# Performance work log

Measured on AMD Instinct MI355X. Metric: run time of the kernel, lower is better.

The kernel has to match this reference:

```python
import jax, jax.numpy as jnp
import numpy as np

NEG = -1e30  # log(0) surrogate that stays finite in fp32
BLANK = 0


def setup_inputs() -> dict:
    key = jax.random.key(0)
    k1, k2 = jax.random.split(key)
    B, T, V, L = 32, 1024, 1024, 256
    logits = jax.random.normal(k1, (B, T, V), dtype=jnp.float32)
    log_probs = jax.nn.log_softmax(logits, axis=-1)  # module expects log-probs
    labels = jax.random.randint(k2, (B, L), 1, V, dtype=jnp.int32)  # avoid blank=0
    input_lens = jnp.full((B,), T, dtype=jnp.int32)
    label_lens = jnp.full((B,), L, dtype=jnp.int32)
    return {"log_probs": log_probs, "labels": labels,
            "input_lens": input_lens, "label_lens": label_lens}


def _ctc_loss_sum(log_probs, labels, input_lens, label_lens, blank=BLANK):
    """CTC forward DP (alpha recursion) in log space; reduction='sum', zero_infinity=True."""
    B, T, V = log_probs.shape
    L = labels.shape[1]
    S = 2 * L + 1  # extended label: blank l1 blank l2 ... blank

    ext = jnp.full((B, S), blank, dtype=labels.dtype)
    ext = ext.at[:, 1::2].set(labels)
    # skip transition s-2 -> s allowed iff ext[s] != blank and ext[s] != ext[s-2]
    skip = jnp.concatenate(
        [jnp.zeros((B, 2), dtype=bool),
         (ext[:, 2:] != blank) & (ext[:, 2:] != ext[:, :-2])], axis=1)

    lp_tbv = jnp.transpose(log_probs, (1, 0, 2))  # 'btv->tbv' as in the module

    emit0 = jnp.take_along_axis(lp_tbv[0], ext, axis=1)  # [B,S]
    alpha0 = jnp.full((B, S), NEG, dtype=log_probs.dtype)
    alpha0 = alpha0.at[:, 0].set(emit0[:, 0]).at[:, 1].set(emit0[:, 1])

    neg1 = jnp.full((B, 1), NEG, dtype=log_probs.dtype)
    neg2 = jnp.full((B, 2), NEG, dtype=log_probs.dtype)

    def step(alpha, inputs):
        lp_t, t = inputs  # lp_t: [B,V]
        em = jnp.take_along_axis(lp_t, ext, axis=1)  # [B,S]
        a1 = alpha
        a2 = jnp.concatenate([neg1, alpha[:, :-1]], axis=1)
        a3 = jnp.where(skip, jnp.concatenate([neg2, alpha[:, :-2]], axis=1), NEG)
        new = jnp.logaddexp(jnp.logaddexp(a1, a2), a3) + em
        # freeze alpha once past this sample's input length
        new = jnp.where((t < input_lens)[:, None], new, alpha)
        return new, None

    ts = jnp.arange(1, T)
    alpha, _ = jax.lax.scan(step, alpha0, (lp_tbv[1:], ts))

    s_last = 2 * label_lens  # final blank state index per sample
    a_last = jnp.take_along_axis(alpha, s_last[:, None], axis=1)[:, 0]
    a_prev = jnp.take_along_axis(alpha, (s_last - 1)[:, None], axis=1)[:, 0]
    loss_b = -jnp.logaddexp(a_last, a_prev)
    loss_b = jnp.where(loss_b > 1e29, 0.0, loss_b)  # zero_infinity=True
    return jnp.sum(loss_b)


def reference(log_probs, labels, input_lens, label_lens):
    return _ctc_loss_sum(log_probs, labels, input_lens, label_lens)
```

## Files before the change

kernel.cpp:

```cpp
#include <hip/hip_runtime.h>


constexpr int B_ = 32, T_ = 1024, V_ = 1024, L_ = 256;
constexpr int CH = 16;
constexpr int NCHUNK = 64;
constexpr int NBUF = 4;
constexpr float LN2F = 0.6931471805599453f;

typedef const __attribute__((address_space(1))) unsigned int* gp_t;
typedef __attribute__((address_space(3))) unsigned int* lp_t;

template <int CTRL>
__device__ __forceinline__ float dpp_fmax(float x) {
    const int t = __builtin_amdgcn_update_dpp(0, __float_as_int(x), CTRL, 0xf, 0xf, true);
    return fmaxf(x, __int_as_float(t));
}

__device__ __forceinline__ float wave_max_dpp(float x) {
    x = dpp_fmax<0x111>(x);
    x = dpp_fmax<0x112>(x);
    x = dpp_fmax<0x114>(x);
    x = dpp_fmax<0x118>(x);
    x = dpp_fmax<0x142>(x);
    x = dpp_fmax<0x143>(x);
    return __int_as_float(__builtin_amdgcn_readlane(__float_as_int(x), 63));
}

__device__ __forceinline__ float dpp_wave_shr1(float x) {
    return __int_as_float(
        __builtin_amdgcn_update_dpp(0, __float_as_int(x), 0x138, 0xf, 0xf, true));
}

__global__ __launch_bounds__(256, 8) void ctc_gather(
    const float* __restrict__ lp, float* __restrict__ qdst, int qstride,
    const int* __restrict__ labels, float* __restrict__ blanks)
{
    __shared__ float srow[4][V_];
    const int wave = threadIdx.x >> 6;
    const int lane = threadIdx.x & 63;
    const int r = blockIdx.x * 4 + wave;
    const int b = r >> 10;
    const float* row = lp + (size_t)r * V_;
    float* orow = qdst + (size_t)r * qstride;
    const int* labb = labels + b * L_;

    #pragma unroll
    for (int j = 0; j < 4; ++j)
        __builtin_amdgcn_global_load_lds((gp_t)(row + 256 * j + 4 * lane),
                                         (lp_t)&srow[wave][256 * j], 16, 0, 0);
    const int4 e = *(const int4*)(labb + 4 * lane);
    asm volatile("s_waitcnt vmcnt(0)" ::: "memory");
    __builtin_amdgcn_sched_barrier(0);
    const float v0 = srow[wave][e.x];
    const float v1 = srow[wave][e.y];
    const float v2 = srow[wave][e.z];
    const float v3 = srow[wave][e.w];
    const float vb = srow[wave][0];
    float4 q;
    q.x = __expf(v0); q.y = __expf(v1); q.z = __expf(v2); q.w = __expf(v3);
    const float qb = __expf(vb);
    *(float4*)(orow + 4 * lane) = q;
    if (lane == 0) {
        const int t = r & (T_ - 1);
        blanks[(r & ~(T_ - 1)) + ((t + T_ - 1) & (T_ - 1))] = qb;
    }
}

__global__ __launch_bounds__(64, 1) void ctc_dp(
    const float* __restrict__ Q, int qstride,
    const float* __restrict__ blanks, const int* __restrict__ labels,
    const int* __restrict__ input_lens, const int* __restrict__ label_lens,
    float* __restrict__ out)
{
    __shared__ float blk[T_];
    __shared__ float buf[NBUF][CH][256];
    const int b    = blockIdx.x;
    const int lane = threadIdx.x & 63;
    const float* Qb  = Q + (size_t)b * T_ * qstride;
    const float* blg = blanks + b * T_;
    const int*  labb = labels + b * L_;
    const int il = input_lens[b];
    const int ll = label_lens[b];
    const int tend = il < T_ ? il : T_;

    auto issue_chunk = [&](int c) {
        #pragma unroll
        for (int i = 0; i < CH; ++i) {
            int t = 1 + c * CH + i; if (t > T_ - 1) t = T_ - 1;
            __builtin_amdgcn_global_load_lds(
                (gp_t)(Qb + (size_t)t * qstride + 4 * lane),
                (lp_t)&buf[c & (NBUF - 1)][i][0], 16, 0, 0);
        }
    };

    #pragma unroll
    for (int i = 0; i < 4; ++i)
        __builtin_amdgcn_global_load_lds((gp_t)(blg + 256 * i + 4 * lane),
                                         (lp_t)&blk[256 * i], 16, 0, 0);
    issue_chunk(0); issue_chunk(1); issue_chunk(2);

    const int4 e  = *(const int4*)(labb + 4 * lane);
    const int  ep = (lane > 0) ? labb[4 * lane - 1] : -1;
    const float kf0 = ((8 * lane + 1) >= 3 && e.x != ep) ? 1.f : 0.f;
    const float kf1 = (e.y != e.x) ? 1.f : 0.f;
    const float kf2 = (e.z != e.y) ? 1.f : 0.f;
    const float kf3 = (e.w != e.z) ? 1.f : 0.f;
    const float bl0 = blg[T_ - 1];
    const float q00 = Qb[0];
    float p0 = (lane == 0) ? bl0 : 0.f;
    float p1 = (lane == 0) ? q00 : 0.f;
    float p2 = 0.f, p3 = 0.f, p4 = 0.f, p5 = 0.f,
          p6 = 0.f, p7 = 0.f, p8 = 0.f;
    int Esc = 0;
    float pm1 = 0.f;
    float sfP = 1.f, sfM = 1.f;

    asm volatile("s_waitcnt vmcnt(32)" ::: "memory");
    __builtin_amdgcn_sched_barrier(0);

    auto snap = [&]() -> float {
        float m = fmaxf(fmaxf(fmaxf(fmaxf(p0, p1), fmaxf(p2, p3)),
                              fmaxf(fmaxf(p4, p5), fmaxf(p6, p7))), p8);
        m = wave_max_dpp(m);
        const unsigned eb = (__float_as_uint(m) >> 23) & 0xffu;
        if (eb >= 1u && eb <= 254u) {
            unsigned k = 318u - eb;
            if (k > 254u) k = 254u;
            Esc += (int)k - 127;
            return __uint_as_float(k << 23);
        }
        return 1.f;
    };

    for (int c = 0; c < NCHUNK; ++c) {
        if (c + 3 < NCHUNK) {
            issue_chunk(c + 3);
            asm volatile("s_waitcnt vmcnt(32)" ::: "memory");
        } else if (c == NCHUNK - 3) {
            asm volatile("s_waitcnt vmcnt(16)" ::: "memory");
        } else if (c == NCHUNK - 2) {
            asm volatile("s_waitcnt vmcnt(0)"  ::: "memory");
        }
        __builtin_amdgcn_sched_barrier(0);

        const float* base = &buf[c & (NBUF - 1)][0][0] + 4 * lane;
        float4 qv[CH];
        #pragma unroll
        for (int i = 0; i < CH; ++i)
            qv[i] = *(const float4*)(base + 256 * i);
        float bb[CH];
        #pragma unroll
        for (int i = 0; i < CH; i += 4) {
            const float4 t4 = *(const float4*)&blk[c * CH + i];
            bb[i] = t4.x; bb[i + 1] = t4.y;
            bb[i + 2] = t4.z; bb[i + 3] = t4.w;
        }
        #pragma unroll
        for (int i = 0; i < CH; ++i) {
            float4 q = qv[i];
            float qb = bb[i];
            if (i == 0) { q.x *= sfP; q.y *= sfP; q.z *= sfP; q.w *= sfP; qb *= sfP; }
            if (i == 8) { q.x *= sfM; q.y *= sfM; q.z *= sfM; q.w *= sfM; qb *= sfM; }
            const int t = 1 + c * CH + i;
            if (t < tend) {
                const float n7 = fmaf(kf3, p5, p7 + p6) * q.w;
                const float n8 = (p8 + p7) * qb;
                const float pm1n = dpp_wave_shr1(n7);
                const float n0 = (p0 + pm1) * qb;
                const float n1 = fmaf(kf0, pm1, p1 + p0) * q.x;
                const float n2 = (p2 + p1) * qb;
                const float n3 = fmaf(kf1, p1, p3 + p2) * q.y;
                const float n4 = (p4 + p3) * qb;
                const float n5 = fmaf(kf2, p3, p5 + p4) * q.z;
                const float n6 = (p6 + p5) * qb;
                p0 = n0; p1 = n1; p2 = n2; p3 = n3; p4 = n4;
                p5 = n5; p6 = n6; p7 = n7; p8 = n8; pm1 = pm1n;
            }
            if (i == 4)  sfM = snap();
            if (i == 12) sfP = snap();
        }
    }
    p0 *= sfP; p1 *= sfP; p2 *= sfP; p3 *= sfP; p4 *= sfP;
    p5 *= sfP; p6 *= sfP; p7 *= sfP; p8 *= sfP;

    const int sl = 2 * ll;
    auto pick = [&](int s) -> float {
        if (s == 512) return __shfl(p8, 63);
        const int r = s & 7;
        float v = p0;
        v = (r == 1) ? p1 : v; v = (r == 2) ? p2 : v;
        v = (r == 3) ? p3 : v; v = (r == 4) ? p4 : v;
        v = (r == 5) ? p5 : v; v = (r == 6) ? p6 : v;
        v = (r == 7) ? p7 : v;
        return __shfl(v, s >> 3);
    };
    const float la = pick(sl);
    const float lb = pick(sl - 1);
    if (lane == 0) {
        const float tot = la + lb;
        float loss = (float)Esc * LN2F - __logf(tot);
        if (!(loss <= 1e29f)) loss = 0.f;
        atomicAdd(out, loss);
    }
}

extern "C" void kernel_launch(void* const* d_in, const int* in_sizes, int n_in,
                              void* d_out, int out_size, void* d_ws, size_t ws_size,
                              hipStream_t stream) {
    float*       lp     = (float*)d_in[0];
    const int*   labels = (const int*)d_in[1];
    const int*   il     = (const int*)d_in[2];
    const int*   ll     = (const int*)d_in[3];
    float* out    = (float*)d_out;
    float* blanks = (float*)d_ws;

    const size_t need = (size_t)B_ * T_ * sizeof(float)
                      + (size_t)B_ * T_ * 256 * sizeof(float);
    const bool use_ws = ws_size >= need;
    float* qdst = use_ws ? (blanks + (size_t)B_ * T_) : lp;
    const int qstride = use_ws ? 256 : V_;

    hipMemsetAsync(out, 0, sizeof(float), stream);
    ctc_gather<<<dim3(B_ * T_ / 4), dim3(256), 0, stream>>>(
        lp, qdst, qstride, labels, blanks);
    ctc_dp<<<dim3(B_), dim3(64), 0, stream>>>(
        qdst, qstride, blanks, labels, il, ll, out);
}
```

Measured before the change: 299.5 us.

## Split DP kernel into producer waves and consumer wave with LDS flag handshake

The DP block grows from one wave to five. Four producer waves load chunks of gathered probabilities from global memory into LDS ring slots, and a single consumer wave runs the serial recurrence, synchronising through workgroup-scope acquire/release flags. This takes the global-load issue and waitcnt stalls off the latency-critical recurrence wave. In exchange it adds spin-wait polling on LDS atomics, register round-trips for the loads instead of direct global-to-LDS transfers, and extra waves competing for issue slots.

```diff
diff --git a/kernel.cpp b/kernel.cpp
--- a/kernel.cpp
+++ b/kernel.cpp
@@ -5,6 +5,7 @@
 constexpr int CH = 16;
 constexpr int NCHUNK = 64;
 constexpr int NBUF = 4;
+constexpr int PROD = 4;
 constexpr float LN2F = 0.6931471805599453f;
 
 typedef const __attribute__((address_space(1))) unsigned int* gp_t;
@@ -66,7 +67,7 @@
     }
 }
 
-__global__ __launch_bounds__(64, 1) void ctc_dp(
+__global__ __launch_bounds__(320, 1) void ctc_dp(
     const float* __restrict__ Q, int qstride,
     const float* __restrict__ blanks, const int* __restrict__ labels,
     const int* __restrict__ input_lens, const int* __restrict__ label_lens,
@@ -74,8 +75,12 @@
 {
     __shared__ float blk[T_];
     __shared__ float buf[NBUF][CH][256];
+    __shared__ int Pf[NBUF];
+    __shared__ int Cf;
     const int b    = blockIdx.x;
-    const int lane = threadIdx.x & 63;
+    const int tid  = threadIdx.x;
+    const int lane = tid & 63;
+    const int wv   = tid >> 6;
     const float* Qb  = Q + (size_t)b * T_ * qstride;
     const float* blg = blanks + b * T_;
     const int*  labb = labels + b * L_;
@@ -83,124 +88,136 @@
     const int ll = label_lens[b];
     const int tend = il < T_ ? il : T_;
 
-    auto issue_chunk = [&](int c) {
+    if (tid < NBUF) Pf[tid] = 0;
+    if (tid == NBUF) Cf = 0;
+    __syncthreads();
+
+    if (wv < PROD) {
+        for (int c = wv; c < NCHUNK; c += PROD) {
+            if (c >= NBUF) {
+                while (__hip_atomic_load(&Cf, __ATOMIC_ACQUIRE,
+                                         __HIP_MEMORY_SCOPE_WORKGROUP)
+                       < c - (NBUF - 1)) {}
+            }
+            float4 r[CH];
+            #pragma unroll
+            for (int i = 0; i < CH; ++i) {
+                int t = 1 + c * CH + i; if (t > T_ - 1) t = T_ - 1;
+                r[i] = *(const float4*)(Qb + (size_t)t * qstride + 4 * lane);
+            }
+            float* dst = &buf[wv][0][0] + 4 * lane;
+            #pragma unroll
+            for (int i = 0; i < CH; ++i)
+                *(float4*)(dst + 256 * i) = r[i];
+            if (lane == 0)
+                __hip_atomic_store(&Pf[wv], c + 1, __ATOMIC_RELEASE,
+                                   __HIP_MEMORY_SCOPE_WORKGROUP);
+        }
+    } else {
         #pragma unroll
-        for (int i = 0; i < CH; ++i) {
-            int t = 1 + c * CH + i; if (t > T_ - 1) t = T_ - 1;
-            __builtin_amdgcn_global_load_lds(
-                (gp_t)(Qb + (size_t)t * qstride + 4 * lane),
-                (lp_t)&buf[c & (NBUF - 1)][i][0], 16, 0, 0);
+        for (int i = 0; i < 4; ++i)
+            __builtin_amdgcn_global_load_lds((gp_t)(blg + 256 * i + 4 * lane),
+                                             (lp_t)&blk[256 * i], 16, 0, 0);
+
+        const int4 e  = *(const int4*)(labb + 4 * lane);
+        const int  ep = (lane > 0) ? labb[4 * lane - 1] : -1;
+        const float kf0 = ((8 * lane + 1) >= 3 && e.x != ep) ? 1.f : 0.f;
+        const float kf1 = (e.y != e.x) ? 1.f : 0.f;
+        const float kf2 = (e.z != e.y) ? 1.f : 0.f;
+        const float kf3 = (e.w != e.z) ? 1.f : 0.f;
+        const float bl0 = blg[T_ - 1];
+        const float q00 = Qb[0];
+        float p0 = (lane == 0) ? bl0 : 0.f;
+        float p1 = (lane == 0) ? q00 : 0.f;
+        float p2 = 0.f, p3 = 0.f, p4 = 0.f, p5 = 0.f,
+              p6 = 0.f, p7 = 0.f, p8 = 0.f;
+        int Esc = 0;
+        float pm1 = 0.f;
+        float sfP = 1.f, sfM = 1.f;
+
+        asm volatile("s_waitcnt vmcnt(0)" ::: "memory");
+        __builtin_amdgcn_sched_barrier(0);
+
+        auto snap = [&]() -> float {
+            float m = fmaxf(fmaxf(fmaxf(fmaxf(p0, p1), fmaxf(p2, p3)),
+                                  fmaxf(fmaxf(p4, p5), fmaxf(p6, p7))), p8);
+            m = wave_max_dpp(m);
+            const unsigned eb = (__float_as_uint(m) >> 23) & 0xffu;
+            if (eb >= 1u && eb <= 254u) {
+                unsigned k = 318u - eb;
+                if (k > 254u) k = 254u;
+                Esc += (int)k - 127;
+                return __uint_as_float(k << 23);
+            }
+            return 1.f;
+        };
+
+        for (int c = 0; c < NCHUNK; ++c) {
+            const int slot = c & (NBUF - 1);
+            while (__hip_atomic_load(&Pf[slot], __ATOMIC_ACQUIRE,
+                                     __HIP_MEMORY_SCOPE_WORKGROUP) < c + 1) {}
+            const float* base = &buf[slot][0][0] + 4 * lane;
+            float4 qv[CH];
+            #pragma unroll
+            for (int i = 0; i < CH; ++i)
+                qv[i] = *(const float4*)(base + 256 * i);
+            float bb[CH];
+            #pragma unroll
+            for (int i = 0; i < CH; i += 4) {
+                const float4 t4 = *(const float4*)&blk[c * CH + i];
+                bb[i] = t4.x; bb[i + 1] = t4.y;
+                bb[i + 2] = t4.z; bb[i + 3] = t4.w;
+            }
+            if (lane == 0)
+                __hip_atomic_store(&Cf, c + 1, __ATOMIC_RELEASE,
+                                   __HIP_MEMORY_SCOPE_WORKGROUP);
+            #pragma unroll
+            for (int i = 0; i < CH; ++i) {
+                float4 q = qv[i];
+                float qb = bb[i];
+                if (i == 0) { q.x *= sfP; q.y *= sfP; q.z *= sfP; q.w *= sfP; qb *= sfP; }
+                if (i == 8) { q.x *= sfM; q.y *= sfM; q.z *= sfM; q.w *= sfM; qb *= sfM; }
+                const int t = 1 + c * CH + i;
+                if (t < tend) {
+                    const float n7 = fmaf(kf3, p5, p7 + p6) * q.w;
+                    const float n8 = (p8 + p7) * qb;
+                    const float pm1n = dpp_wave_shr1(n7);
+                    const float n0 = (p0 + pm1) * qb;
+                    const float n1 = fmaf(kf0, pm1, p1 + p0) * q.x;
+                    const float n2 = (p2 + p1) * qb;
+                    const float n3 = fmaf(kf1, p1, p3 + p2) * q.y;
+                    const float n4 = (p4 + p3) * qb;
+                    const float n5 = fmaf(kf2, p3, p5 + p4) * q.z;
+                    const float n6 = (p6 + p5) * qb;
+                    p0 = n0; p1 = n1; p2 = n2; p3 = n3; p4 = n4;
+                    p5 = n5; p6 = n6; p7 = n7; p8 = n8; pm1 = pm1n;
+                }
+                if (i == 4)  sfM = snap();
+                if (i == 12) sfP = snap();
+            }
         }
-    };
-
-    #pragma unroll
-    for (int i = 0; i < 4; ++i)
-        __builtin_amdgcn_global_load_lds((gp_t)(blg + 256 * i + 4 * lane),
-                                         (lp_t)&blk[256 * i], 16, 0, 0);
-    issue_chunk(0); issue_chunk(1); issue_chunk(2);
-
-    const int4 e  = *(const int4*)(labb + 4 * lane);
-    const int  ep = (lane > 0) ? labb[4 * lane - 1] : -1;
-    const float kf0 = ((8 * lane + 1) >= 3 && e.x != ep) ? 1.f : 0.f;
-    const float kf1 = (e.y != e.x) ? 1.f : 0.f;
-    const float kf2 = (e.z != e.y) ? 1.f : 0.f;
-    const float kf3 = (e.w != e.z) ? 1.f : 0.f;
-    const float bl0 = blg[T_ - 1];
-    const float q00 = Qb[0];
-    float p0 = (lane == 0) ? bl0 : 0.f;
-    float p1 = (lane == 0) ? q00 : 0.f;
-    float p2 = 0.f, p3 = 0.f, p4 = 0.f, p5 = 0.f,
-          p6 = 0.f, p7 = 0.f, p8 = 0.f;
-    int Esc = 0;
-    float pm1 = 0.f;
-    float sfP = 1.f, sfM = 1.f;
-
-    asm volatile("s_waitcnt vmcnt(32)" ::: "memory");
-    __builtin_amdgcn_sched_barrier(0);
-
-    auto snap = [&]() -> float {
-        float m = fmaxf(fmaxf(fmaxf(fmaxf(p0, p1), fmaxf(p2, p3)),
-                              fmaxf(fmaxf(p4, p5), fmaxf(p6, p7))), p8);
-        m = wave_max_dpp(m);
-        const unsigned eb = (__float_as_uint(m) >> 23) & 0xffu;
-        if (eb >= 1u && eb <= 254u) {
-            unsigned k = 318u - eb;
-            if (k > 254u) k = 254u;
-            Esc += (int)k - 127;
-            return __uint_as_float(k << 23);
+        p0 *= sfP; p1 *= sfP; p2 *= sfP; p3 *= sfP; p4 *= sfP;
+        p5 *= sfP; p6 *= sfP; p7 *= sfP; p8 *= sfP;
+
+        const int sl = 2 * ll;
+        auto pick = [&](int s) -> float {
+            if (s == 512) return __shfl(p8, 63);
+            const int r = s & 7;
+            float v = p0;
+            v = (r == 1) ? p1 : v; v = (r == 2) ? p2 : v;
+            v = (r == 3) ? p3 : v; v = (r == 4) ? p4 : v;
+            v = (r == 5) ? p5 : v; v = (r == 6) ? p6 : v;
+            v = (r == 7) ? p7 : v;
+            return __shfl(v, s >> 3);
+        };
+        const float la = pick(sl);
+        const float lb = pick(sl - 1);
+        if (lane == 0) {
+            const float tot = la + lb;
+            float loss = (float)Esc * LN2F - __logf(tot);
+            if (!(loss <= 1e29f)) loss = 0.f;
+            atomicAdd(out, loss);
         }
-        return 1.f;
-    };
-
-    for (int c = 0; c < NCHUNK; ++c) {
-        if (c + 3 < NCHUNK) {
-            issue_chunk(c + 3);
-            asm volatile("s_waitcnt vmcnt(32)" ::: "memory");
-        } else if (c == NCHUNK - 3) {
-            asm volatile("s_waitcnt vmcnt(16)" ::: "memory");
-        } else if (c == NCHUNK - 2) {
-            asm volatile("s_waitcnt vmcnt(0)"  ::: "memory");
-        }
-        __builtin_amdgcn_sched_barrier(0);
-
-        const float* base = &buf[c & (NBUF - 1)][0][0] + 4 * lane;
-        float4 qv[CH];
-        #pragma unroll
-        for (int i = 0; i < CH; ++i)
-            qv[i] = *(const float4*)(base + 256 * i);
-        float bb[CH];
-        #pragma unroll
-        for (int i = 0; i < CH; i += 4) {
-            const float4 t4 = *(const float4*)&blk[c * CH + i];
-            bb[i] = t4.x; bb[i + 1] = t4.y;
-            bb[i + 2] = t4.z; bb[i + 3] = t4.w;
-        }
-        #pragma unroll
-        for (int i = 0; i < CH; ++i) {
-            float4 q = qv[i];
-            float qb = bb[i];
-            if (i == 0) { q.x *= sfP; q.y *= sfP; q.z *= sfP; q.w *= sfP; qb *= sfP; }
-            if (i == 8) { q.x *= sfM; q.y *= sfM; q.z *= sfM; q.w *= sfM; qb *= sfM; }
-            const int t = 1 + c * CH + i;
-            if (t < tend) {
-                const float n7 = fmaf(kf3, p5, p7 + p6) * q.w;
-                const float n8 = (p8 + p7) * qb;
-                const float pm1n = dpp_wave_shr1(n7);
-                const float n0 = (p0 + pm1) * qb;
-                const float n1 = fmaf(kf0, pm1, p1 + p0) * q.x;
-                const float n2 = (p2 + p1) * qb;
-                const float n3 = fmaf(kf1, p1, p3 + p2) * q.y;
-                const float n4 = (p4 + p3) * qb;
-                const float n5 = fmaf(kf2, p3, p5 + p4) * q.z;
-                const float n6 = (p6 + p5) * qb;
-                p0 = n0; p1 = n1; p2 = n2; p3 = n3; p4 = n4;
-                p5 = n5; p6 = n6; p7 = n7; p8 = n8; pm1 = pm1n;
-            }
-            if (i == 4)  sfM = snap();
-            if (i == 12) sfP = snap();
-        }
-    }
-    p0 *= sfP; p1 *= sfP; p2 *= sfP; p3 *= sfP; p4 *= sfP;
-    p5 *= sfP; p6 *= sfP; p7 *= sfP; p8 *= sfP;
-
-    const int sl = 2 * ll;
-    auto pick = [&](int s) -> float {
-        if (s == 512) return __shfl(p8, 63);
-        const int r = s & 7;
-        float v = p0;
-        v = (r == 1) ? p1 : v; v = (r == 2) ? p2 : v;
-        v = (r == 3) ? p3 : v; v = (r == 4) ? p4 : v;
-        v = (r == 5) ? p5 : v; v = (r == 6) ? p6 : v;
-        v = (r == 7) ? p7 : v;
-        return __shfl(v, s >> 3);
-    };
-    const float la = pick(sl);
-    const float lb = pick(sl - 1);
-    if (lane == 0) {
-        const float tot = la + lb;
-        float loss = (float)Esc * LN2F - __logf(tot);
-        if (!(loss <= 1e29f)) loss = 0.f;
-        atomicAdd(out, loss);
     }
 }
 
@@ -223,6 +240,6 @@
     hipMemsetAsync(out, 0, sizeof(float), stream);
     ctc_gather<<<dim3(B_ * T_ / 4), dim3(256), 0, stream>>>(
         lp, qdst, qstride, labels, blanks);
-    ctc_dp<<<dim3(B_), dim3(64), 0, stream>>>(
+    ctc_dp<<<dim3(B_), dim3(320), 0, stream>>>(
         qdst, qstride, blanks, labels, il, ll, out);
 }
```

New measurement: 302.7 us. About the same (+1.1%).

## Stage DP chunks through registers with double-buffered LDS and explicit ds_reads

Applied to the files above, without the earlier changes.

Replaces the 4-deep async global-to-LDS prefetch in the serial CTC DP kernel with register-staged global loads of the next chunk, written into a 2-slot LDS buffer after each chunk's compute. Per-step operands are fetched with explicit inline-asm ds_read_b128 in two batches of 8, each followed by a single lgkmcnt wait. The aim is tighter control of LDS read latency and instruction scheduling in the latency-bound recurrence. In exchange, prefetch depth drops to one chunk, about 64 extra VGPRs hold the staged data, and a full vmcnt(0) wait sits at the end of every chunk.

```diff
diff --git a/kernel.cpp b/kernel.cpp
--- a/kernel.cpp
+++ b/kernel.cpp
@@ -4,7 +4,6 @@
 constexpr int B_ = 32, T_ = 1024, V_ = 1024, L_ = 256;
 constexpr int CH = 16;
 constexpr int NCHUNK = 64;
-constexpr int NBUF = 4;
 constexpr float LN2F = 0.6931471805599453f;
 
 typedef const __attribute__((address_space(1))) unsigned int* gp_t;
@@ -66,6 +65,14 @@
     }
 }
 
+#define GL16(dst, t_expr)                                                   \
+    { int t_ = (t_expr); if (t_ > T_ - 1) t_ = T_ - 1;                      \
+      const float* p_ = Qb + (size_t)t_ * qstride + 4 * lane;               \
+      asm volatile("global_load_dwordx4 %0, %1, off"                        \
+                   : "=&v"(dst) : "v"(p_)); }
+#define DSR(dst, addr)                                                      \
+    asm volatile("ds_read_b128 %0, %1" : "=&v"(dst) : "v"(addr))
+
 __global__ __launch_bounds__(64, 1) void ctc_dp(
     const float* __restrict__ Q, int qstride,
     const float* __restrict__ blanks, const int* __restrict__ labels,
@@ -73,7 +80,7 @@
     float* __restrict__ out)
 {
     __shared__ float blk[T_];
-    __shared__ float buf[NBUF][CH][256];
+    __shared__ float buf[2][CH][256];
     const int b    = blockIdx.x;
     const int lane = threadIdx.x & 63;
     const float* Qb  = Q + (size_t)b * T_ * qstride;
@@ -83,21 +90,10 @@
     const int ll = label_lens[b];
     const int tend = il < T_ ? il : T_;
 
-    auto issue_chunk = [&](int c) {
-        #pragma unroll
-        for (int i = 0; i < CH; ++i) {
-            int t = 1 + c * CH + i; if (t > T_ - 1) t = T_ - 1;
-            __builtin_amdgcn_global_load_lds(
-                (gp_t)(Qb + (size_t)t * qstride + 4 * lane),
-                (lp_t)&buf[c & (NBUF - 1)][i][0], 16, 0, 0);
-        }
-    };
-
     #pragma unroll
     for (int i = 0; i < 4; ++i)
         __builtin_amdgcn_global_load_lds((gp_t)(blg + 256 * i + 4 * lane),
                                          (lp_t)&blk[256 * i], 16, 0, 0);
-    issue_chunk(0); issue_chunk(1); issue_chunk(2);
 
     const int4 e  = *(const int4*)(labb + 4 * lane);
     const int  ep = (lane > 0) ? labb[4 * lane - 1] : -1;
@@ -115,8 +111,9 @@
     float pm1 = 0.f;
     float sfP = 1.f, sfM = 1.f;
 
-    asm volatile("s_waitcnt vmcnt(32)" ::: "memory");
-    __builtin_amdgcn_sched_barrier(0);
+    const unsigned bufb = (unsigned)(size_t)(lp_t)&buf[0][0][0];
+    const unsigned blkb = (unsigned)(size_t)(lp_t)&blk[0];
+    const unsigned lane16 = (unsigned)lane * 16u;
 
     auto snap = [&]() -> float {
         float m = fmaxf(fmaxf(fmaxf(fmaxf(p0, p1), fmaxf(p2, p3)),
@@ -132,54 +129,111 @@
         return 1.f;
     };
 
+    float4 r0, r1, r2, r3, r4, r5, r6, r7,
+           r8, r9, r10, r11, r12, r13, r14, r15;
+    float4 qv0, qv1, qv2, qv3, qv4, qv5, qv6, qv7;
+    float4 bb0, bb1, bb2, bb3;
+
+#define STORE_CHUNK(slot_)                                                  \
+    {                                                                       \
+        float* wb_ = &buf[(slot_)][0][0] + 4 * lane;                        \
+        *(float4*)(wb_ + 0 * 256)  = r0;  *(float4*)(wb_ + 1 * 256)  = r1;  \
+        *(float4*)(wb_ + 2 * 256)  = r2;  *(float4*)(wb_ + 3 * 256)  = r3;  \
+        *(float4*)(wb_ + 4 * 256)  = r4;  *(float4*)(wb_ + 5 * 256)  = r5;  \
+        *(float4*)(wb_ + 6 * 256)  = r6;  *(float4*)(wb_ + 7 * 256)  = r7;  \
+        *(float4*)(wb_ + 8 * 256)  = r8;  *(float4*)(wb_ + 9 * 256)  = r9;  \
+        *(float4*)(wb_ + 10 * 256) = r10; *(float4*)(wb_ + 11 * 256) = r11; \
+        *(float4*)(wb_ + 12 * 256) = r12; *(float4*)(wb_ + 13 * 256) = r13; \
+        *(float4*)(wb_ + 14 * 256) = r14; *(float4*)(wb_ + 15 * 256) = r15; \
+    }
+
+    GL16(r0, 1);  GL16(r1, 2);  GL16(r2, 3);  GL16(r3, 4);
+    GL16(r4, 5);  GL16(r5, 6);  GL16(r6, 7);  GL16(r7, 8);
+    GL16(r8, 9);  GL16(r9, 10); GL16(r10, 11); GL16(r11, 12);
+    GL16(r12, 13); GL16(r13, 14); GL16(r14, 15); GL16(r15, 16);
+    asm volatile("s_waitcnt vmcnt(0)" ::: "memory");
+    __builtin_amdgcn_sched_barrier(0);
+    STORE_CHUNK(0);
+    asm volatile("s_waitcnt lgkmcnt(0)" ::: "memory");
+    __builtin_amdgcn_sched_barrier(0);
+
+#define DP_STEP(ii, qvec)                                                   \
+    {                                                                       \
+        float4 q = (qvec);                                                  \
+        const float4 f4 = ((ii) >> 2) == 0 ? bb0 : ((ii) >> 2) == 1 ? bb1   \
+                        : ((ii) >> 2) == 2 ? bb2 : bb3;                     \
+        const int g = (ii) & 3;                                             \
+        float qb = (g == 0) ? f4.x : (g == 1) ? f4.y                        \
+                 : (g == 2) ? f4.z : f4.w;                                  \
+        if ((ii) == 0) { q.x *= sfP; q.y *= sfP; q.z *= sfP; q.w *= sfP;    \
+                         qb *= sfP; }                                       \
+        if ((ii) == 8) { q.x *= sfM; q.y *= sfM; q.z *= sfM; q.w *= sfM;    \
+                         qb *= sfM; }                                       \
+        const int t = 1 + c * CH + (ii);                                    \
+        if (t < tend) {                                                     \
+            const float n7 = fmaf(kf3, p5, p7 + p6) * q.w;                  \
+            const float n8 = (p8 + p7) * qb;                                \
+            const float pm1n = dpp_wave_shr1(n7);                           \
+            const float n0 = (p0 + pm1) * qb;                               \
+            const float n1 = fmaf(kf0, pm1, p1 + p0) * q.x;                 \
+            const float n2 = (p2 + p1) * qb;                                \
+            const float n3 = fmaf(kf1, p1, p3 + p2) * q.y;                  \
+            const float n4 = (p4 + p3) * qb;                                \
+            const float n5 = fmaf(kf2, p3, p5 + p4) * q.z;                  \
+            const float n6 = (p6 + p5) * qb;                                \
+            p0 = n0; p1 = n1; p2 = n2; p3 = n3; p4 = n4;                    \
+            p5 = n5; p6 = n6; p7 = n7; p8 = n8; pm1 = pm1n;                 \
+        }                                                                   \
+        if ((ii) == 4)  sfM = snap();                                       \
+        if ((ii) == 12) sfP = snap();                                       \
+    }
+
     for (int c = 0; c < NCHUNK; ++c) {
-        if (c + 3 < NCHUNK) {
-            issue_chunk(c + 3);
-            asm volatile("s_waitcnt vmcnt(32)" ::: "memory");
-        } else if (c == NCHUNK - 3) {
-            asm volatile("s_waitcnt vmcnt(16)" ::: "memory");
-        } else if (c == NCHUNK - 2) {
-            asm volatile("s_waitcnt vmcnt(0)"  ::: "memory");
+        const bool more = (c + 1 < NCHUNK);
+        if (more) {
+            const int tb = 1 + (c + 1) * CH;
+            GL16(r0, tb + 0);  GL16(r1, tb + 1);  GL16(r2, tb + 2);
+            GL16(r3, tb + 3);  GL16(r4, tb + 4);  GL16(r5, tb + 5);
+            GL16(r6, tb + 6);  GL16(r7, tb + 7);  GL16(r8, tb + 8);
+            GL16(r9, tb + 9);  GL16(r10, tb + 10); GL16(r11, tb + 11);
+            GL16(r12, tb + 12); GL16(r13, tb + 13); GL16(r14, tb + 14);
+            GL16(r15, tb + 15);
         }
+        const unsigned qa0 = bufb + ((unsigned)(c & 1) << 14) + lane16;
+        DSR(qv0, qa0 + 0u * 1024u); DSR(qv1, qa0 + 1u * 1024u);
+        DSR(qv2, qa0 + 2u * 1024u); DSR(qv3, qa0 + 3u * 1024u);
+        DSR(qv4, qa0 + 4u * 1024u); DSR(qv5, qa0 + 5u * 1024u);
+        DSR(qv6, qa0 + 6u * 1024u); DSR(qv7, qa0 + 7u * 1024u);
+        const unsigned ba0 = blkb + (unsigned)c * 64u;
+        DSR(bb0, ba0 + 0u); DSR(bb1, ba0 + 16u);
+        DSR(bb2, ba0 + 32u); DSR(bb3, ba0 + 48u);
+        asm volatile("s_waitcnt lgkmcnt(0)" ::: "memory");
         __builtin_amdgcn_sched_barrier(0);
 
-        const float* base = &buf[c & (NBUF - 1)][0][0] + 4 * lane;
-        float4 qv[CH];
-        #pragma unroll
-        for (int i = 0; i < CH; ++i)
-            qv[i] = *(const float4*)(base + 256 * i);
-        float bb[CH];
-        #pragma unroll
-        for (int i = 0; i < CH; i += 4) {
-            const float4 t4 = *(const float4*)&blk[c * CH + i];
-            bb[i] = t4.x; bb[i + 1] = t4.y;
-            bb[i + 2] = t4.z; bb[i + 3] = t4.w;
+        DP_STEP(0, qv0) DP_STEP(1, qv1) DP_STEP(2, qv2) DP_STEP(3, qv3)
+        DP_STEP(4, qv4) DP_STEP(5, qv5) DP_STEP(6, qv6) DP_STEP(7, qv7)
+
+        DSR(qv0, qa0 + 8u * 1024u);  DSR(qv1, qa0 + 9u * 1024u);
+        DSR(qv2, qa0 + 10u * 1024u); DSR(qv3, qa0 + 11u * 1024u);
+        DSR(qv4, qa0 + 12u * 1024u); DSR(qv5, qa0 + 13u * 1024u);
+        DSR(qv6, qa0 + 14u * 1024u); DSR(qv7, qa0 + 15u * 1024u);
+        asm volatile("s_waitcnt lgkmcnt(0)" ::: "memory");
+        __builtin_amdgcn_sched_barrier(0);
+
+        DP_STEP(8, qv0)  DP_STEP(9, qv1)  DP_STEP(10, qv2) DP_STEP(11, qv3)
+        DP_STEP(12, qv4) DP_STEP(13, qv5) DP_STEP(14, qv6) DP_STEP(15, qv7)
+
+        if (more) {
+            asm volatile("s_waitcnt vmcnt(0)" ::: "memory");
+            __builtin_amdgcn_sched_barrier(0);
+            STORE_CHUNK((c + 1) & 1);
+            asm volatile("s_waitcnt lgkmcnt(0)" ::: "memory");
+            __builtin_amdgcn_sched_barrier(0);
         }
-        #pragma unroll
-        for (int i = 0; i < CH; ++i) {
-            float4 q = qv[i];
-            float qb = bb[i];
-            if (i == 0) { q.x *= sfP; q.y *= sfP; q.z *= sfP; q.w *= sfP; qb *= sfP; }
-            if (i == 8) { q.x *= sfM; q.y *= sfM; q.z *= sfM; q.w *= sfM; qb *= sfM; }
-            const int t = 1 + c * CH + i;
-            if (t < tend) {
-                const float n7 = fmaf(kf3, p5, p7 + p6) * q.w;
-                const float n8 = (p8 + p7) * qb;
-                const float pm1n = dpp_wave_shr1(n7);
-                const float n0 = (p0 + pm1) * qb;
-                const float n1 = fmaf(kf0, pm1, p1 + p0) * q.x;
-                const float n2 = (p2 + p1) * qb;
-                const float n3 = fmaf(kf1, p1, p3 + p2) * q.y;
-                const float n4 = (p4 + p3) * qb;
-                const float n5 = fmaf(kf2, p3, p5 + p4) * q.z;
-                const float n6 = (p6 + p5) * qb;
-                p0 = n0; p1 = n1; p2 = n2; p3 = n3; p4 = n4;
-                p5 = n5; p6 = n6; p7 = n7; p8 = n8; pm1 = pm1n;
-            }
-            if (i == 4)  sfM = snap();
-            if (i == 12) sfP = snap();
-        }
-    }
+    }
+#undef DP_STEP
+#undef STORE_CHUNK
+
     p0 *= sfP; p1 *= sfP; p2 *= sfP; p3 *= sfP; p4 *= sfP;
     p5 *= sfP; p6 *= sfP; p7 *= sfP; p8 *= sfP;
 
```

Result: slower. 414.9 us (+38.5%).
